# Performance work log

Measured on AMD Instinct MI355X. Metric: run time of the kernel, lower is better.

The kernel has to match this reference:

```python
import jax, jax.numpy as jnp
import numpy as np

B, IN, H = 8192, 512, 2048
DT, TAU_FAST, TAU_SLOW, MEM_TAU = 10.0, 200.0, 1500.0, 100.0
DT_SEC = DT / 1000.0          # 0.01
ALPHA_NEURON = DT / MEM_TAU   # 0.1


def _stsp_buffers(h):
    num_exc = int(np.round(h * 0.8))
    ei = np.ones(h, dtype=np.float32)
    ei[num_exc:] = -1.0
    alpha_stf = np.empty((1, h), np.float32)
    alpha_std = np.empty((1, h), np.float32)
    U = np.empty((1, h), np.float32)
    # exc -> depressing, inh -> facilitating ('exc_dep_inh_fac')
    dep = ei == 1.0
    alpha_stf[0, dep] = DT / TAU_FAST
    alpha_std[0, dep] = DT / TAU_SLOW
    U[0, dep] = 0.45
    alpha_stf[0, ~dep] = DT / TAU_SLOW
    alpha_std[0, ~dep] = DT / TAU_FAST
    U[0, ~dep] = 0.15
    dyn = np.ones((1, h), np.float32)
    mask = (np.ones((h, h)) - np.eye(h)).astype(np.float32)
    return ei, alpha_stf, alpha_std, U, dyn, mask


def setup_inputs() -> dict:
    key = jax.random.key(0)
    ks = jax.random.split(key, 6)
    ei, a_stf, a_std, U, dyn, mask = _stsp_buffers(H)
    rng = np.random.default_rng(0)
    w_ih = np.float32(rng.gamma(0.2, 1.0, size=(IN, H)))
    w_hh = np.float32(rng.gamma(1.0, 1.0, size=(H, H))) * mask
    num_inh = H - int(np.round(H * 0.8))
    return {
        "inp": jax.random.uniform(ks[0], (B, IN), jnp.float32),
        "h_in": jax.random.uniform(ks[1], (B, H), jnp.float32),
        "syn_x": jax.random.uniform(ks[2], (B, H), jnp.float32),
        "syn_u": jax.random.uniform(ks[3], (B, H), jnp.float32),
        "weight_ih": jnp.asarray(w_ih),
        "weight_hh": jnp.asarray(w_hh),
        "bias": jnp.zeros((H,), jnp.float32),
        "alpha_stf": jnp.asarray(a_stf),
        "alpha_std": jnp.asarray(a_std),
        "U": jnp.asarray(U),
        "dynamic_synapse": jnp.asarray(dyn),
        "EI_vec": jnp.asarray(ei),
        "w_mask": jnp.asarray(mask),
    }


def reference(inp, h_in, syn_x, syn_u, weight_ih, weight_hh, bias,
              alpha_stf, alpha_std, U, dynamic_synapse, EI_vec, w_mask):
    # STSP state updates (use pre-update syn_x/syn_u, then clamp)
    syn_x_new = syn_x + (alpha_std * (1.0 - syn_x) - DT_SEC * syn_u * syn_x * h_in) * dynamic_synapse
    syn_u_new = syn_u + (alpha_stf * (U - syn_u) + DT_SEC * U * (1.0 - syn_u) * h_in) * dynamic_synapse
    syn_x_new = jnp.clip(syn_x_new, 0.0, 1.0)
    syn_u_new = jnp.clip(syn_u_new, 0.0, 1.0)
    h_post = syn_u_new * syn_x_new * h_in  # [B, H]
    # EI-constrained recurrent weights: diag(EI) @ relu(W) with zeroed diagonal
    eff_w = w_mask * (EI_vec[:, None] * jax.nn.relu(weight_hh))
    pre = jnp.matmul(inp, jax.nn.relu(weight_ih)) + jnp.matmul(h_post, eff_w) + bias
    h_out = h_in * (1.0 - ALPHA_NEURON) + ALPHA_NEURON * jax.nn.relu(pre)
    return h_out, syn_x_new, syn_u_new
```

## Files before the change

### kernel.cpp

```cpp
#include <hip/hip_runtime.h>
#include <hip/hip_bf16.h>
#include <stdint.h>

#define NB 8192
#define NIN 512
#define NH 2048
#define NK (NIN + NH)
#define NT (NK / 64)

typedef __bf16 bf16;
typedef __bf16 bf16x4 __attribute__((ext_vector_type(4)));
typedef __bf16 bf16x8 __attribute__((ext_vector_type(8)));
typedef float  f32x4  __attribute__((ext_vector_type(4)));

__device__ __forceinline__ void gload16(const void* g, void* l) {
    __builtin_amdgcn_global_load_lds(
        (const __attribute__((address_space(1))) void*)g,
        (__attribute__((address_space(3))) void*)l, 16, 0, 0);
}

#define FENCE()      asm volatile("" ::: "memory")
#define BAR()        do { FENCE(); __builtin_amdgcn_s_barrier(); FENCE(); } while (0)
#define WAIT_LGKM0() asm volatile("s_waitcnt lgkmcnt(0)" ::: "memory")
#define WAIT_LGKM8() asm volatile("s_waitcnt lgkmcnt(8)" ::: "memory")
#define WAIT_VM(n)   asm volatile("s_waitcnt vmcnt(" #n ")" ::: "memory")

__global__ void ew_kernel(const float* __restrict__ h_in,
                          const float* __restrict__ syn_x,
                          const float* __restrict__ syn_u,
                          const float* __restrict__ a_stf,
                          const float* __restrict__ a_std,
                          const float* __restrict__ Uv,
                          const float* __restrict__ dyn,
                          float* __restrict__ out_sx,
                          float* __restrict__ out_su,
                          bf16* __restrict__ Abuf)
{
    int t = blockIdx.x * blockDim.x + threadIdx.x;
    int e = t * 4;
    int row = e >> 11;
    int col = e & 2047;
    f32x4 h    = *(const f32x4*)&h_in[e];
    f32x4 sx   = *(const f32x4*)&syn_x[e];
    f32x4 su   = *(const f32x4*)&syn_u[e];
    f32x4 astf = *(const f32x4*)&a_stf[col];
    f32x4 astd = *(const f32x4*)&a_std[col];
    f32x4 Uq   = *(const f32x4*)&Uv[col];
    f32x4 dq   = *(const f32x4*)&dyn[col];
    f32x4 nsx, nsu;
    bf16x4 hpb;
#pragma unroll
    for (int i = 0; i < 4; ++i) {
        float x = sx[i] + (astd[i] * (1.0f - sx[i]) - 0.01f * su[i] * sx[i] * h[i]) * dq[i];
        float u = su[i] + (astf[i] * (Uq[i] - su[i]) + 0.01f * Uq[i] * (1.0f - su[i]) * h[i]) * dq[i];
        x = fminf(fmaxf(x, 0.0f), 1.0f);
        u = fminf(fmaxf(u, 0.0f), 1.0f);
        nsx[i] = x;
        nsu[i] = u;
        hpb[i] = (bf16)(u * x * h[i]);
    }
    *(f32x4*)&out_sx[e] = nsx;
    *(f32x4*)&out_su[e] = nsu;
    *(bf16x4*)&Abuf[(size_t)row * NK + NIN + col] = hpb;
}

__global__ void conv_inp(const float* __restrict__ inp, bf16* __restrict__ Abuf)
{
    int t = blockIdx.x * blockDim.x + threadIdx.x;
    int e = t * 4;
    int row = e >> 9;
    int col = e & 511;
    f32x4 v = *(const f32x4*)&inp[e];
    bf16x4 b;
#pragma unroll
    for (int i = 0; i < 4; ++i) b[i] = (bf16)v[i];
    *(bf16x4*)&Abuf[(size_t)row * NK + col] = b;
}

__global__ void prep_w(const float* __restrict__ w_ih,
                       const float* __restrict__ w_hh,
                       const float* __restrict__ w_mask,
                       const float* __restrict__ EI,
                       bf16* __restrict__ Bt)
{
    __shared__ float tile[32][33];
    int b  = blockIdx.x;
    int tk = b % (NK / 32);
    int tn = b / (NK / 32);
    int k0 = tk * 32, n0 = tn * 32;
    int t  = threadIdx.x;
    int lc = t & 31;
    int lr = t >> 5;
#pragma unroll
    for (int it = 0; it < 4; ++it) {
        int kr = lr + it * 8;
        int k  = k0 + kr;
        int n  = n0 + lc;
        float v;
        if (k < NIN) {
            v = fmaxf(w_ih[(size_t)k * NH + n], 0.0f);
        } else {
            int i = k - NIN;
            float w = fmaxf(w_hh[(size_t)i * NH + n], 0.0f);
            v = w_mask[(size_t)i * NH + n] * EI[i] * w;
        }
        tile[kr][lc] = v;
    }
    __syncthreads();
#pragma unroll
    for (int it = 0; it < 4; ++it) {
        int nr = lr + it * 8;
        Bt[(size_t)(n0 + nr) * NK + k0 + lc] = (bf16)tile[lc][nr];
    }
}

__global__ __launch_bounds__(512, 2)
void gemm_fused(const bf16* __restrict__ A,
                const bf16* __restrict__ Bt,
                const float* __restrict__ h_in,
                const float* __restrict__ bias,
                float* __restrict__ h_out)
{
    __shared__ bf16 sA[2][16384];
    __shared__ bf16 sB[2][16384];

    const int bid  = blockIdx.x;
    const int bid2 = (bid & 7) * 32 + (bid >> 3);
    const int tm = bid2 >> 3, tn = bid2 & 7;
    const int rowBase = tm * 256, colBase = tn * 256;

    const int tid  = threadIdx.x;
    const int wid  = tid >> 6, lane = tid & 63;
    const int wr   = wid >> 2, wc = wid & 3;
    const int ln15 = lane & 15, l4 = lane >> 4;

    const int sr  = lane >> 3;
    const int gcs = (((lane & 7) ^ sr) << 3);
    const int sk0 = ((l4 ^ (ln15 & 7)) << 3);
    const int sk1 = sk0 ^ 32;

    f32x4 acc[8][4];
#pragma unroll
    for (int i = 0; i < 8; ++i)
#pragma unroll
        for (int j = 0; j < 4; ++j) acc[i][j] = (f32x4){0.f, 0.f, 0.f, 0.f};

    bf16x8 af[4][2], bf0[2][2], bf1[2][2];

    auto stA = [&](bf16* dst, int T, int u) {
#pragma unroll
        for (int w = 0; w < 2; ++w) {
            int gr = rowBase + w * 128 + u * 64 + wid * 8 + sr;
            gload16(A + (size_t)gr * NK + T * 64 + gcs,
                    dst + u * 8192 + w * 4096 + wid * 512);
        }
    };
    auto stB = [&](bf16* dst, int T, int u) {
#pragma unroll
        for (int w = 0; w < 2; ++w) {
            int gn = colBase + (w * 2 + (wid >> 2)) * 64 + u * 32 + (wid & 3) * 8 + sr;
            gload16(Bt + (size_t)gn * NK + T * 64 + gcs,
                    dst + u * 8192 + w * 4096 + wid * 512);
        }
    };

#define READ_A(MH) do {                                                        \
    const bf16* _ba = &sAc[(MH) * 8192 + wr * 4096 + ln15 * 64];               \
    _Pragma("unroll") for (int m = 0; m < 4; ++m) {                            \
        af[m][0] = *(const bf16x8*)(_ba + m * 1024 + sk0);                     \
        af[m][1] = *(const bf16x8*)(_ba + m * 1024 + sk1); } } while (0)

#define READ_B(NHALF, bfr) do {                                                \
    const bf16* _bb = &sBc[(NHALF) * 8192 + wc * 2048 + ln15 * 64];            \
    _Pragma("unroll") for (int n = 0; n < 2; ++n) {                            \
        bfr[n][0] = *(const bf16x8*)(_bb + n * 1024 + sk0);                    \
        bfr[n][1] = *(const bf16x8*)(_bb + n * 1024 + sk1); } } while (0)

#define MFMA16(MH, NHALF, bfr) do {                                            \
    __builtin_amdgcn_s_setprio(1);                                             \
    _Pragma("unroll") for (int kk = 0; kk < 2; ++kk)                           \
    _Pragma("unroll") for (int m = 0; m < 4; ++m)                              \
    _Pragma("unroll") for (int n = 0; n < 2; ++n)                              \
        acc[(MH) * 4 + m][(NHALF) * 2 + n] =                                   \
            __builtin_amdgcn_mfma_f32_16x16x32_bf16(                           \
                af[m][kk], bfr[n][kk], acc[(MH) * 4 + m][(NHALF) * 2 + n],     \
                0, 0, 0);                                                      \
    __builtin_amdgcn_s_setprio(0); } while (0)

#define TILE(t, sAc_, sBc_, sAn_, sBn_, S1, S2, VMW) do {                      \
    const bf16* sAc = sAc_; const bf16* sBc = sBc_;                            \
                                                                       \
    READ_A(0); READ_B(0, bf0);                                                 \
    if (S1) stA(sAn_, (t) + 1, 1);                                             \
    WAIT_LGKM8();                                                              \
    BAR(); WAIT_LGKM0(); MFMA16(0, 0, bf0); BAR();                             \
                                                                       \
    READ_B(1, bf1);                                                            \
    if (S2) stA((bf16*)sAc_, (t) + 2, 0);                                      \
    BAR(); WAIT_LGKM0(); MFMA16(0, 1, bf1); BAR();                             \
                                                                       \
    READ_A(1);                                                                 \
    if (S2) stB((bf16*)sBc_, (t) + 2, 0);                                      \
    BAR(); WAIT_LGKM0(); MFMA16(1, 1, bf1); BAR();                             \
                     \
    if (S2) stB((bf16*)sBc_, (t) + 2, 1);                                      \
    MFMA16(1, 0, bf0);                                                         \
    VMW;                                                                       \
    BAR(); } while (0)

    stA(sA[0], 0, 0); stB(sB[0], 0, 0); stA(sA[0], 0, 1); stB(sB[0], 0, 1);
    stA(sA[1], 1, 0); stB(sB[1], 1, 0); stB(sB[1], 1, 1);
    WAIT_VM(6);
    BAR();

    for (int t = 0; t < NT - 2; t += 2) {
        TILE(t,     sA[0], sB[0], sA[1], sB[1], 1, 1, WAIT_VM(6));
        TILE(t + 1, sA[1], sB[1], sA[0], sB[0], 1, 1, WAIT_VM(6));
    }
    TILE(NT - 2, sA[0], sB[0], sA[1], sB[1], 1, 0, WAIT_VM(0));
    TILE(NT - 1, sA[1], sB[1], sA[0], sB[0], 0, 0, FENCE());

#pragma unroll
    for (int mf = 0; mf < 8; ++mf) {
#pragma unroll
        for (int nf = 0; nf < 4; ++nf) {
            int col = colBase + wc * 64 + nf * 16 + ln15;
            float bv = bias[col];
            int row0 = rowBase + wr * 128 + mf * 16 + l4 * 4;
#pragma unroll
            for (int r = 0; r < 4; ++r) {
                size_t idx = (size_t)(row0 + r) * NH + col;
                float pre = acc[mf][nf][r] + bv;
                h_out[idx] = 0.9f * h_in[idx] + 0.1f * fmaxf(pre, 0.0f);
            }
        }
    }
#undef READ_A
#undef READ_B
#undef MFMA16
#undef TILE
}

extern "C" void kernel_launch(void* const* d_in, const int* in_sizes, int n_in,
                              void* d_out, int out_size, void* d_ws, size_t ws_size,
                              hipStream_t stream)
{
    const float* inp    = (const float*)d_in[0];
    const float* h_in   = (const float*)d_in[1];
    const float* syn_x  = (const float*)d_in[2];
    const float* syn_u  = (const float*)d_in[3];
    const float* w_ih   = (const float*)d_in[4];
    const float* w_hh   = (const float*)d_in[5];
    const float* bias   = (const float*)d_in[6];
    const float* a_stf  = (const float*)d_in[7];
    const float* a_std  = (const float*)d_in[8];
    const float* Uv     = (const float*)d_in[9];
    const float* dyn    = (const float*)d_in[10];
    const float* EI     = (const float*)d_in[11];
    const float* w_mask = (const float*)d_in[12];

    float* out   = (float*)d_out;
    float* out_h = out;
    float* out_x = out + (size_t)NB * NH;
    float* out_u = out + 2 * (size_t)NB * NH;

    bf16* Abuf = (bf16*)d_ws;
    bf16* Btw  = Abuf + (size_t)NB * NK;

    ew_kernel<<<(NB * NH) / (256 * 4), 256, 0, stream>>>(
        h_in, syn_x, syn_u, a_stf, a_std, Uv, dyn, out_x, out_u, Abuf);
    conv_inp<<<(NB * NIN) / (256 * 4), 256, 0, stream>>>(inp, Abuf);
    prep_w<<<(NK / 32) * (NH / 32), 256, 0, stream>>>(w_ih, w_hh, w_mask, EI, Btw);
    gemm_fused<<<(NB / 256) * (NH / 256), 512, 0, stream>>>(Abuf, Btw, h_in, bias, out_h);
}
```

Measured before the change: 184.1 us.

## Restructure GEMM tile schedule to batch LDS reads and merge elementwise kernels

The GEMM main loop now issues all A and B fragment LDS reads for a k-tile up front into a doubled A-fragment register array. It then uses graded lgkmcnt waits so MFMAs can start before all reads land, and cuts the barriers per tile from seven to two, moving the next-tile global loads after a single barrier. Separately, the input-conversion kernel is merged into the elementwise STSP kernel via a block-index branch, saving one launch. Holding more fragments raises register pressure, and the fewer barriers change how LDS reuse is protected.

New measurement: 208.4 us. 13.2% more time.

```diff
diff --git a/kernel.cpp b/kernel.cpp
--- a/kernel.cpp
+++ b/kernel.cpp
@@ -21,10 +21,11 @@
 
 #define FENCE()      asm volatile("" ::: "memory")
 #define BAR()        do { FENCE(); __builtin_amdgcn_s_barrier(); FENCE(); } while (0)
-#define WAIT_LGKM0() asm volatile("s_waitcnt lgkmcnt(0)" ::: "memory")
-#define WAIT_LGKM8() asm volatile("s_waitcnt lgkmcnt(8)" ::: "memory")
+#define WAIT_LGKM(n) asm volatile("s_waitcnt lgkmcnt(" #n ")" ::: "memory")
 #define WAIT_VM(n)   asm volatile("s_waitcnt vmcnt(" #n ")" ::: "memory")
 
+#define EW_BLK ((NB * NH) / (256 * 4))
+#define CV_BLK ((NB * NIN) / (256 * 4))
 __global__ void ew_kernel(const float* __restrict__ h_in,
                           const float* __restrict__ syn_x,
                           const float* __restrict__ syn_u,
@@ -32,49 +33,49 @@
                           const float* __restrict__ a_std,
                           const float* __restrict__ Uv,
                           const float* __restrict__ dyn,
+                          const float* __restrict__ inp,
                           float* __restrict__ out_sx,
                           float* __restrict__ out_su,
                           bf16* __restrict__ Abuf)
 {
-    int t = blockIdx.x * blockDim.x + threadIdx.x;
-    int e = t * 4;
-    int row = e >> 11;
-    int col = e & 2047;
-    f32x4 h    = *(const f32x4*)&h_in[e];
-    f32x4 sx   = *(const f32x4*)&syn_x[e];
-    f32x4 su   = *(const f32x4*)&syn_u[e];
-    f32x4 astf = *(const f32x4*)&a_stf[col];
-    f32x4 astd = *(const f32x4*)&a_std[col];
-    f32x4 Uq   = *(const f32x4*)&Uv[col];
-    f32x4 dq   = *(const f32x4*)&dyn[col];
-    f32x4 nsx, nsu;
-    bf16x4 hpb;
-#pragma unroll
-    for (int i = 0; i < 4; ++i) {
-        float x = sx[i] + (astd[i] * (1.0f - sx[i]) - 0.01f * su[i] * sx[i] * h[i]) * dq[i];
-        float u = su[i] + (astf[i] * (Uq[i] - su[i]) + 0.01f * Uq[i] * (1.0f - su[i]) * h[i]) * dq[i];
-        x = fminf(fmaxf(x, 0.0f), 1.0f);
-        u = fminf(fmaxf(u, 0.0f), 1.0f);
-        nsx[i] = x;
-        nsu[i] = u;
-        hpb[i] = (bf16)(u * x * h[i]);
-    }
-    *(f32x4*)&out_sx[e] = nsx;
-    *(f32x4*)&out_su[e] = nsu;
-    *(bf16x4*)&Abuf[(size_t)row * NK + NIN + col] = hpb;
-}
-
-__global__ void conv_inp(const float* __restrict__ inp, bf16* __restrict__ Abuf)
-{
-    int t = blockIdx.x * blockDim.x + threadIdx.x;
-    int e = t * 4;
-    int row = e >> 9;
-    int col = e & 511;
-    f32x4 v = *(const f32x4*)&inp[e];
-    bf16x4 b;
-#pragma unroll
-    for (int i = 0; i < 4; ++i) b[i] = (bf16)v[i];
-    *(bf16x4*)&Abuf[(size_t)row * NK + col] = b;
+    if (blockIdx.x < EW_BLK) {
+        int t = blockIdx.x * blockDim.x + threadIdx.x;
+        int e = t * 4;
+        int row = e >> 11;
+        int col = e & 2047;
+        f32x4 h    = *(const f32x4*)&h_in[e];
+        f32x4 sx   = *(const f32x4*)&syn_x[e];
+        f32x4 su   = *(const f32x4*)&syn_u[e];
+        f32x4 astf = *(const f32x4*)&a_stf[col];
+        f32x4 astd = *(const f32x4*)&a_std[col];
+        f32x4 Uq   = *(const f32x4*)&Uv[col];
+        f32x4 dq   = *(const f32x4*)&dyn[col];
+        f32x4 nsx, nsu;
+        bf16x4 hpb;
+#pragma unroll
+        for (int i = 0; i < 4; ++i) {
+            float x = sx[i] + (astd[i] * (1.0f - sx[i]) - 0.01f * su[i] * sx[i] * h[i]) * dq[i];
+            float u = su[i] + (astf[i] * (Uq[i] - su[i]) + 0.01f * Uq[i] * (1.0f - su[i]) * h[i]) * dq[i];
+            x = fminf(fmaxf(x, 0.0f), 1.0f);
+            u = fminf(fmaxf(u, 0.0f), 1.0f);
+            nsx[i] = x;
+            nsu[i] = u;
+            hpb[i] = (bf16)(u * x * h[i]);
+        }
+        *(f32x4*)&out_sx[e] = nsx;
+        *(f32x4*)&out_su[e] = nsu;
+        *(bf16x4*)&Abuf[(size_t)row * NK + NIN + col] = hpb;
+    } else {
+        int t = (blockIdx.x - EW_BLK) * blockDim.x + threadIdx.x;
+        int e = t * 4;
+        int row = e >> 9;
+        int col = e & 511;
+        f32x4 v = *(const f32x4*)&inp[e];
+        bf16x4 b;
+#pragma unroll
+        for (int i = 0; i < 4; ++i) b[i] = (bf16)v[i];
+        *(bf16x4*)&Abuf[(size_t)row * NK + col] = b;
+    }
 }
 
 __global__ void prep_w(const float* __restrict__ w_ih,
@@ -145,7 +146,7 @@
 #pragma unroll
         for (int j = 0; j < 4; ++j) acc[i][j] = (f32x4){0.f, 0.f, 0.f, 0.f};
 
-    bf16x8 af[4][2], bf0[2][2], bf1[2][2];
+    bf16x8 af[8][2], bf0[2][2], bf1[2][2];
 
     auto stA = [&](bf16* dst, int T, int u) {
 #pragma unroll
@@ -167,8 +168,8 @@
 #define READ_A(MH) do {                                                        \
     const bf16* _ba = &sAc[(MH) * 8192 + wr * 4096 + ln15 * 64];               \
     _Pragma("unroll") for (int m = 0; m < 4; ++m) {                            \
-        af[m][0] = *(const bf16x8*)(_ba + m * 1024 + sk0);                     \
-        af[m][1] = *(const bf16x8*)(_ba + m * 1024 + sk1); } } while (0)
+        af[(MH) * 4 + m][0] = *(const bf16x8*)(_ba + m * 1024 + sk0);          \
+        af[(MH) * 4 + m][1] = *(const bf16x8*)(_ba + m * 1024 + sk1); } } while (0)
 
 #define READ_B(NHALF, bfr) do {                                                \
     const bf16* _bb = &sBc[(NHALF) * 8192 + wc * 2048 + ln15 * 64];            \
@@ -176,39 +177,42 @@
         bfr[n][0] = *(const bf16x8*)(_bb + n * 1024 + sk0);                    \
         bfr[n][1] = *(const bf16x8*)(_bb + n * 1024 + sk1); } } while (0)
 
-#define MFMA16(MH, NHALF, bfr) do {                                            \
-    __builtin_amdgcn_s_setprio(1);                                             \
+#define MFMAQ(MH, NHALF, bfr) do {                                             \
     _Pragma("unroll") for (int kk = 0; kk < 2; ++kk)                           \
     _Pragma("unroll") for (int m = 0; m < 4; ++m)                              \
     _Pragma("unroll") for (int n = 0; n < 2; ++n)                              \
         acc[(MH) * 4 + m][(NHALF) * 2 + n] =                                   \
             __builtin_amdgcn_mfma_f32_16x16x32_bf16(                           \
-                af[m][kk], bfr[n][kk], acc[(MH) * 4 + m][(NHALF) * 2 + n],     \
-                0, 0, 0);                                                      \
-    __builtin_amdgcn_s_setprio(0); } while (0)
+                af[(MH) * 4 + m][kk], bfr[n][kk],                              \
+                acc[(MH) * 4 + m][(NHALF) * 2 + n], 0, 0, 0);                  \
+    } while (0)
 
 #define TILE(t, sAc_, sBc_, sAn_, sBn_, S1, S2, VMW) do {                      \
     const bf16* sAc = sAc_; const bf16* sBc = sBc_;                            \
-                                                                       \
-    READ_A(0); READ_B(0, bf0);                                                 \
-    if (S1) stA(sAn_, (t) + 1, 1);                                             \
-    WAIT_LGKM8();                                                              \
-    BAR(); WAIT_LGKM0(); MFMA16(0, 0, bf0); BAR();                             \
-                                                                       \
-    READ_B(1, bf1);                                                            \
-    if (S2) stA((bf16*)sAc_, (t) + 2, 0);                                      \
-    BAR(); WAIT_LGKM0(); MFMA16(0, 1, bf1); BAR();                             \
-                                                                       \
-    READ_A(1);                                                                 \
-    if (S2) stB((bf16*)sBc_, (t) + 2, 0);                                      \
-    BAR(); WAIT_LGKM0(); MFMA16(1, 1, bf1); BAR();                             \
-                     \
-    if (S2) stB((bf16*)sBc_, (t) + 2, 1);                                      \
-    MFMA16(1, 0, bf0);                                                         \
+         \
+    READ_A(0); READ_B(0, bf0); FENCE();                                        \
+    READ_B(1, bf1); FENCE();                                                   \
+    READ_A(1); FENCE();                                                        \
+    if (S1) stA(sAn_, (t) + 1, 1);  \
+    WAIT_LGKM(12);                                             \
+    __builtin_amdgcn_s_setprio(1);                                             \
+    MFMAQ(0, 0, bf0);                                                          \
+    WAIT_LGKM(8);                                                 \
+    MFMAQ(0, 1, bf1);                                                          \
+    __builtin_amdgcn_s_setprio(0);                                             \
+    WAIT_LGKM(0);                                     \
+    BAR();            \
+    if (S2) { stA((bf16*)sAc_, (t) + 2, 0);                                    \
+              stB((bf16*)sBc_, (t) + 2, 0);                                    \
+              stB((bf16*)sBc_, (t) + 2, 1); }                                  \
+    __builtin_amdgcn_s_setprio(1);                                             \
+    MFMAQ(1, 1, bf1);                                                          \
+    MFMAQ(1, 0, bf0);                                                          \
+    __builtin_amdgcn_s_setprio(0);                                             \
     VMW;                                                                       \
     BAR(); } while (0)
 
-    stA(sA[0], 0, 0); stB(sB[0], 0, 0); stA(sA[0], 0, 1); stB(sB[0], 0, 1);
+    stA(sA[0], 0, 0); stB(sB[0], 0, 0); stB(sB[0], 0, 1); stA(sA[0], 0, 1);
     stA(sA[1], 1, 0); stB(sB[1], 1, 0); stB(sB[1], 1, 1);
     WAIT_VM(6);
     BAR();
@@ -237,7 +241,7 @@
     }
 #undef READ_A
 #undef READ_B
-#undef MFMA16
+#undef MFMAQ
 #undef TILE
 }
 
@@ -267,9 +271,8 @@
     bf16* Abuf = (bf16*)d_ws;
     bf16* Btw  = Abuf + (size_t)NB * NK;
 
-    ew_kernel<<<(NB * NH) / (256 * 4), 256, 0, stream>>>(
-        h_in, syn_x, syn_u, a_stf, a_std, Uv, dyn, out_x, out_u, Abuf);
-    conv_inp<<<(NB * NIN) / (256 * 4), 256, 0, stream>>>(inp, Abuf);
+    ew_kernel<<<EW_BLK + CV_BLK, 256, 0, stream>>>(
+        h_in, syn_x, syn_u, a_stf, a_std, Uv, dyn, inp, out_x, out_u, Abuf);
     prep_w<<<(NK / 32) * (NH / 32), 256, 0, stream>>>(w_ih, w_hh, w_mask, EI, Btw);
     gemm_fused<<<(NB / 256) * (NH / 256), 512, 0, stream>>>(Abuf, Btw, h_in, bias, out_h);
 }
```
